# Kernel optimization log

Measured on AMD Instinct MI355X. Metric: run time of the kernel, lower is better.

Reference implementation:

```python
import jax, jax.numpy as jnp
import numpy as np
from jax import lax

BN_EPS = 1e-3  # keras BatchNormalization default
DN = ('NHWC', 'HWIO', 'NHWC')


def setup_inputs() -> dict:
    key = jax.random.key(0)
    ks = jax.random.split(key, 8)
    B, H, W, C = 16, 224, 224, 96
    K = 3
    x = jax.random.normal(ks[0], (B, H, W, C), dtype=jnp.float32)
    dw_kernel = jax.random.normal(ks[1], (K, K, 1, C), dtype=jnp.float32) * 0.1
    dw_bias = jnp.zeros((C,), dtype=jnp.float32)
    pw_kernel = jax.random.normal(ks[2], (1, 1, C, C), dtype=jnp.float32) * 0.1
    pw_bias = jnp.zeros((C,), dtype=jnp.float32)
    gamma = jax.random.uniform(ks[3], (C,), dtype=jnp.float32, minval=0.5, maxval=1.5)
    beta = jax.random.normal(ks[4], (C,), dtype=jnp.float32) * 0.1
    moving_mean = jax.random.normal(ks[5], (C,), dtype=jnp.float32) * 0.1
    moving_var = jax.random.uniform(ks[6], (C,), dtype=jnp.float32, minval=0.5, maxval=1.5)
    return {
        'x': x, 'dw_kernel': dw_kernel, 'dw_bias': dw_bias,
        'pw_kernel': pw_kernel, 'pw_bias': pw_bias,
        'gamma': gamma, 'beta': beta,
        'moving_mean': moving_mean, 'moving_var': moving_var,
    }


def reference(x, dw_kernel, dw_bias, pw_kernel, pw_bias, gamma, beta, moving_mean, moving_var):
    C = x.shape[-1]
    stride = 1
    # ReLU at the start of the op
    y = jax.nn.relu(x)
    # Depthwise conv: feature_group_count = C, kernel HWIO = (K, K, 1, C)
    y = lax.conv_general_dilated(
        y, dw_kernel, window_strides=(stride, stride), padding='SAME',
        dimension_numbers=DN, feature_group_count=C)
    y = y + dw_bias
    # Pointwise 1x1 conv to C_curr channels
    y = lax.conv_general_dilated(
        y, pw_kernel, window_strides=(1, 1), padding='SAME',
        dimension_numbers=DN)
    y = y + pw_bias
    # BatchNormalization (inference mode: use moving statistics)
    inv = gamma * lax.rsqrt(moving_var + BN_EPS)
    y = y * inv + (beta - moving_mean * inv)
    return y
```

## Files before the change

kernel.cpp:

```cpp
#include <hip/hip_runtime.h>
#include <hip/hip_bf16.h>


#define BATCH 16
#define HH 224
#define WWD 224
#define CC 96
#define ROWS (BATCH*HH)
#define TPR 14
#define NTILES (ROWS*TPR)
#define NTHREADS 256
#define WAVES 4
#define NBLOCKS 1024
#define NXCD 8
#define TILES_PER_BAND (NTILES/NXCD)
#define WAVES_PER_BAND ((NBLOCKS/NXCD)*WAVES)
#define PAD 104

typedef __attribute__((ext_vector_type(8))) short short8;
typedef __attribute__((ext_vector_type(4))) float f32x4;

__device__ __forceinline__ unsigned short f2bf(float f){
    union{float f; unsigned u;} v; v.f = f;
    unsigned r = v.u + 0x7fffu + ((v.u >> 16) & 1u);
    return (unsigned short)(r >> 16);
}

__device__ __forceinline__ void tap_fma(const float* __restrict__ xp,
                                        const float* wp,
                                        float acc[3][8])
{
    #pragma unroll
    for (int ks = 0; ks < 3; ++ks) {
        float4 x0 = *reinterpret_cast<const float4*>(xp + ks*32);
        float4 x1 = *reinterpret_cast<const float4*>(xp + ks*32 + 4);
        float4 w0 = *reinterpret_cast<const float4*>(wp + ks*32);
        float4 w1 = *reinterpret_cast<const float4*>(wp + ks*32 + 4);
        acc[ks][0] += fmaxf(x0.x, 0.f) * w0.x;
        acc[ks][1] += fmaxf(x0.y, 0.f) * w0.y;
        acc[ks][2] += fmaxf(x0.z, 0.f) * w0.z;
        acc[ks][3] += fmaxf(x0.w, 0.f) * w0.w;
        acc[ks][4] += fmaxf(x1.x, 0.f) * w1.x;
        acc[ks][5] += fmaxf(x1.y, 0.f) * w1.y;
        acc[ks][6] += fmaxf(x1.z, 0.f) * w1.z;
        acc[ks][7] += fmaxf(x1.w, 0.f) * w1.w;
    }
}

__global__ __launch_bounds__(NTHREADS, 4) void sepconv_kernel(
    const float* __restrict__ x,
    const float* __restrict__ dwk,
    const float* __restrict__ dwb,
    const float* __restrict__ pwk,
    const float* __restrict__ pwb,
    const float* __restrict__ gma,
    const float* __restrict__ bta,
    const float* __restrict__ mmean,
    const float* __restrict__ mvar,
    float* __restrict__ out)
{
    __shared__ __align__(16) unsigned short s_pwT[CC][PAD];
    __shared__ __align__(16) float s_dwk[9][CC];
    __shared__ __align__(16) float s_dwb[CC];
    __shared__ __align__(16) float s_scale[CC];
    __shared__ __align__(16) float s_shift[CC];

    const int t = threadIdx.x;

    for (int e = t; e < CC*CC; e += NTHREADS) {
        int ci = e / CC;
        int co = e - ci*CC;
        s_pwT[co][ci] = f2bf(pwk[e]);
    }
    for (int e = t; e < 9*CC; e += NTHREADS)
        (&s_dwk[0][0])[e] = dwk[e];
    if (t < CC) {
        s_dwb[t] = dwb[t];
        float sc = gma[t] / sqrtf(mvar[t] + 1e-3f);
        s_scale[t] = sc;
        s_shift[t] = (pwb[t] - mmean[t]) * sc + bta[t];
    }
    __syncthreads();

    const int wave = t >> 6;
    const int lane = t & 63;
    const int col  = lane & 15;
    const int quad = lane >> 4;

    float scv[6], shv[6];
    #pragma unroll
    for (int nt = 0; nt < 6; ++nt) {
        scv[nt] = s_scale[nt*16 + col];
        shv[nt] = s_shift[nt*16 + col];
    }

    const int xcd = blockIdx.x & (NXCD-1);
    const int lb  = blockIdx.x >> 3;
    const int gw  = lb*WAVES + wave;
    const int Tend = (xcd+1)*TILES_PER_BAND;

    for (int T = xcd*TILES_PER_BAND + gw; T < Tend; T += WAVES_PER_BAND) {
        const int rrow = T / TPR;
        const int wt   = T - rrow*TPR;
        const int h    = rrow % HH;
        const int w_me = wt*16 + col;
        const float* xb = x + (size_t)(rrow*WWD + w_me)*CC + quad*8;

        float acc[3][8];
        #pragma unroll
        for (int ks = 0; ks < 3; ++ks) {
            float4 b0 = *reinterpret_cast<const float4*>(&s_dwb[ks*32 + quad*8]);
            float4 b1 = *reinterpret_cast<const float4*>(&s_dwb[ks*32 + quad*8 + 4]);
            acc[ks][0]=b0.x; acc[ks][1]=b0.y; acc[ks][2]=b0.z; acc[ks][3]=b0.w;
            acc[ks][4]=b1.x; acc[ks][5]=b1.y; acc[ks][6]=b1.z; acc[ks][7]=b1.w;
        }

        #pragma unroll
        for (int kh = -1; kh <= 1; ++kh) {
            const int h2 = h + kh;
            if ((unsigned)h2 >= HH) continue;
            const float* rp = xb + kh*(WWD*CC);
            const float* wr = &s_dwk[(kh+1)*3][0] + quad*8;
            if (w_me >= 1)       tap_fma(rp - CC, wr,        acc);
                                 tap_fma(rp,      wr + CC,   acc);
            if (w_me <= WWD-2)   tap_fma(rp + CC, wr + 2*CC, acc);
        }

        short8 afr[3];
        #pragma unroll
        for (int ks = 0; ks < 3; ++ks) {
            union { short8 v; unsigned u[4]; } pk;
            #pragma unroll
            for (int j = 0; j < 4; ++j)
                pk.u[j] = (unsigned)f2bf(acc[ks][2*j])
                        | ((unsigned)f2bf(acc[ks][2*j+1]) << 16);
            afr[ks] = pk.v;
        }

        float* ob = out + (size_t)(T*16 + quad*4)*CC + col;
        #pragma unroll
        for (int nt = 0; nt < 6; ++nt) {
            f32x4 macc = {0.f, 0.f, 0.f, 0.f};
            #pragma unroll
            for (int ks = 0; ks < 3; ++ks) {
                short8 bfr = *reinterpret_cast<const short8*>(
                    &s_pwT[nt*16 + col][ks*32 + quad*8]);
                macc = __builtin_amdgcn_mfma_f32_16x16x32_bf16(afr[ks], bfr, macc, 0, 0, 0);
            }
            #pragma unroll
            for (int r2 = 0; r2 < 4; ++r2)
                ob[r2*CC + nt*16] = macc[r2]*scv[nt] + shv[nt];
        }
    }
}

extern "C" void kernel_launch(void* const* d_in, const int* in_sizes, int n_in,
                              void* d_out, int out_size, void* d_ws, size_t ws_size,
                              hipStream_t stream)
{
    sepconv_kernel<<<NBLOCKS, NTHREADS, 0, stream>>>(
        (const float*)d_in[0],
        (const float*)d_in[1],
        (const float*)d_in[2],
        (const float*)d_in[3],
        (const float*)d_in[4],
        (const float*)d_in[5],
        (const float*)d_in[6],
        (const float*)d_in[7],
        (const float*)d_in[8],
        (float*)d_out);
}
```

Measured before the change: 755.6 us.

## Split weight prep into separate kernel and launch one wave per tile

Moves the bf16 transpose of the pointwise weights and the BN scale/shift folding into a small prep kernel that writes to workspace. The main kernel drops its persistent grid-stride loop and launches one block per four tiles, one tile per wave, with occupancy raised to eight blocks per CU. The MFMA operands are swapped so each lane holds four consecutive output channels, which allows float4 stores. Pointwise weights are now read from global memory or cache instead of LDS, which adds global loads per tile, and many more blocks each reload the depthwise weights into LDS.

```diff
diff --git a/kernel.cpp b/kernel.cpp
--- a/kernel.cpp
+++ b/kernel.cpp
@@ -10,12 +10,8 @@
 #define TPR 14
 #define NTILES (ROWS*TPR)
 #define NTHREADS 256
-#define WAVES 4
-#define NBLOCKS 1024
-#define NXCD 8
-#define TILES_PER_BAND (NTILES/NXCD)
-#define WAVES_PER_BAND ((NBLOCKS/NXCD)*WAVES)
-#define PAD 104
+#define NBLOCKS (NTILES/4)
+#define BLK_PER_BAND (NBLOCKS/8)
 
 typedef __attribute__((ext_vector_type(8))) short short8;
 typedef __attribute__((ext_vector_type(4))) float f32x4;
@@ -47,39 +43,43 @@
     }
 }
 
-__global__ __launch_bounds__(NTHREADS, 4) void sepconv_kernel(
+__global__ void sepconv_prep(const float* __restrict__ pwk,
+                             const float* __restrict__ pwb,
+                             const float* __restrict__ gma,
+                             const float* __restrict__ bta,
+                             const float* __restrict__ mmean,
+                             const float* __restrict__ mvar,
+                             unsigned short* __restrict__ pwT,
+                             float* __restrict__ bnsc,
+                             float* __restrict__ bnsh)
+{
+    int e = blockIdx.x*256 + threadIdx.x;
+    int ci = e / CC;
+    int co = e - ci*CC;
+    pwT[co*CC + ci] = f2bf(pwk[e]);
+    if (e < CC) {
+        float sc = gma[e] / sqrtf(mvar[e] + 1e-3f);
+        bnsc[e] = sc;
+        bnsh[e] = (pwb[e] - mmean[e]) * sc + bta[e];
+    }
+}
+
+__global__ __launch_bounds__(NTHREADS, 8) void sepconv_main(
     const float* __restrict__ x,
     const float* __restrict__ dwk,
     const float* __restrict__ dwb,
-    const float* __restrict__ pwk,
-    const float* __restrict__ pwb,
-    const float* __restrict__ gma,
-    const float* __restrict__ bta,
-    const float* __restrict__ mmean,
-    const float* __restrict__ mvar,
+    const unsigned short* __restrict__ pwT,
+    const float* __restrict__ bnsc,
+    const float* __restrict__ bnsh,
     float* __restrict__ out)
 {
-    __shared__ __align__(16) unsigned short s_pwT[CC][PAD];
     __shared__ __align__(16) float s_dwk[9][CC];
     __shared__ __align__(16) float s_dwb[CC];
-    __shared__ __align__(16) float s_scale[CC];
-    __shared__ __align__(16) float s_shift[CC];
 
     const int t = threadIdx.x;
-
-    for (int e = t; e < CC*CC; e += NTHREADS) {
-        int ci = e / CC;
-        int co = e - ci*CC;
-        s_pwT[co][ci] = f2bf(pwk[e]);
-    }
     for (int e = t; e < 9*CC; e += NTHREADS)
         (&s_dwk[0][0])[e] = dwk[e];
-    if (t < CC) {
-        s_dwb[t] = dwb[t];
-        float sc = gma[t] / sqrtf(mvar[t] + 1e-3f);
-        s_scale[t] = sc;
-        s_shift[t] = (pwb[t] - mmean[t]) * sc + bta[t];
-    }
+    if (t < CC) s_dwb[t] = dwb[t];
     __syncthreads();
 
     const int wave = t >> 6;
@@ -87,70 +87,65 @@
     const int col  = lane & 15;
     const int quad = lane >> 4;
 
-    float scv[6], shv[6];
+    const int xcd = blockIdx.x & 7;
+    const int idx = blockIdx.x >> 3;
+    const int T   = (xcd*BLK_PER_BAND + idx)*4 + wave;
+
+    const int rrow = T / TPR;
+    const int wt   = T - rrow*TPR;
+    const int h    = rrow % HH;
+    const int w_me = wt*16 + col;
+    const float* xb = x + (size_t)(rrow*WWD + w_me)*CC + quad*8;
+
+    float acc[3][8];
+    #pragma unroll
+    for (int ks = 0; ks < 3; ++ks) {
+        float4 b0 = *reinterpret_cast<const float4*>(&s_dwb[ks*32 + quad*8]);
+        float4 b1 = *reinterpret_cast<const float4*>(&s_dwb[ks*32 + quad*8 + 4]);
+        acc[ks][0]=b0.x; acc[ks][1]=b0.y; acc[ks][2]=b0.z; acc[ks][3]=b0.w;
+        acc[ks][4]=b1.x; acc[ks][5]=b1.y; acc[ks][6]=b1.z; acc[ks][7]=b1.w;
+    }
+
+    #pragma unroll
+    for (int kh = -1; kh <= 1; ++kh) {
+        const int h2 = h + kh;
+        if ((unsigned)h2 >= HH) continue;
+        const float* rp = xb + kh*(WWD*CC);
+        const float* wr = &s_dwk[(kh+1)*3][0] + quad*8;
+        if (w_me >= 1)       tap_fma(rp - CC, wr,        acc);
+                             tap_fma(rp,      wr + CC,   acc);
+        if (w_me <= WWD-2)   tap_fma(rp + CC, wr + 2*CC, acc);
+    }
+
+    short8 bfr[3];
+    #pragma unroll
+    for (int ks = 0; ks < 3; ++ks) {
+        union { short8 v; unsigned u[4]; } pk;
+        #pragma unroll
+        for (int j = 0; j < 4; ++j)
+            pk.u[j] = (unsigned)f2bf(acc[ks][2*j])
+                    | ((unsigned)f2bf(acc[ks][2*j+1]) << 16);
+        bfr[ks] = pk.v;
+    }
+
+    float* ob = out + (size_t)(T*16 + col)*CC;
     #pragma unroll
     for (int nt = 0; nt < 6; ++nt) {
-        scv[nt] = s_scale[nt*16 + col];
-        shv[nt] = s_shift[nt*16 + col];
-    }
-
-    const int xcd = blockIdx.x & (NXCD-1);
-    const int lb  = blockIdx.x >> 3;
-    const int gw  = lb*WAVES + wave;
-    const int Tend = (xcd+1)*TILES_PER_BAND;
-
-    for (int T = xcd*TILES_PER_BAND + gw; T < Tend; T += WAVES_PER_BAND) {
-        const int rrow = T / TPR;
-        const int wt   = T - rrow*TPR;
-        const int h    = rrow % HH;
-        const int w_me = wt*16 + col;
-        const float* xb = x + (size_t)(rrow*WWD + w_me)*CC + quad*8;
-
-        float acc[3][8];
+        f32x4 macc = {0.f, 0.f, 0.f, 0.f};
         #pragma unroll
         for (int ks = 0; ks < 3; ++ks) {
-            float4 b0 = *reinterpret_cast<const float4*>(&s_dwb[ks*32 + quad*8]);
-            float4 b1 = *reinterpret_cast<const float4*>(&s_dwb[ks*32 + quad*8 + 4]);
-            acc[ks][0]=b0.x; acc[ks][1]=b0.y; acc[ks][2]=b0.z; acc[ks][3]=b0.w;
-            acc[ks][4]=b1.x; acc[ks][5]=b1.y; acc[ks][6]=b1.z; acc[ks][7]=b1.w;
+            short8 pfr = *reinterpret_cast<const short8*>(
+                pwT + (size_t)(nt*16 + col)*CC + ks*32 + quad*8);
+            macc = __builtin_amdgcn_mfma_f32_16x16x32_bf16(pfr, bfr[ks], macc, 0, 0, 0);
         }
-
-        #pragma unroll
-        for (int kh = -1; kh <= 1; ++kh) {
-            const int h2 = h + kh;
-            if ((unsigned)h2 >= HH) continue;
-            const float* rp = xb + kh*(WWD*CC);
-            const float* wr = &s_dwk[(kh+1)*3][0] + quad*8;
-            if (w_me >= 1)       tap_fma(rp - CC, wr,        acc);
-                                 tap_fma(rp,      wr + CC,   acc);
-            if (w_me <= WWD-2)   tap_fma(rp + CC, wr + 2*CC, acc);
-        }
-
-        short8 afr[3];
-        #pragma unroll
-        for (int ks = 0; ks < 3; ++ks) {
-            union { short8 v; unsigned u[4]; } pk;
-            #pragma unroll
-            for (int j = 0; j < 4; ++j)
-                pk.u[j] = (unsigned)f2bf(acc[ks][2*j])
-                        | ((unsigned)f2bf(acc[ks][2*j+1]) << 16);
-            afr[ks] = pk.v;
-        }
-
-        float* ob = out + (size_t)(T*16 + quad*4)*CC + col;
-        #pragma unroll
-        for (int nt = 0; nt < 6; ++nt) {
-            f32x4 macc = {0.f, 0.f, 0.f, 0.f};
-            #pragma unroll
-            for (int ks = 0; ks < 3; ++ks) {
-                short8 bfr = *reinterpret_cast<const short8*>(
-                    &s_pwT[nt*16 + col][ks*32 + quad*8]);
-                macc = __builtin_amdgcn_mfma_f32_16x16x32_bf16(afr[ks], bfr, macc, 0, 0, 0);
-            }
-            #pragma unroll
-            for (int r2 = 0; r2 < 4; ++r2)
-                ob[r2*CC + nt*16] = macc[r2]*scv[nt] + shv[nt];
-        }
+        float4 sc4 = *reinterpret_cast<const float4*>(bnsc + nt*16 + quad*4);
+        float4 sh4 = *reinterpret_cast<const float4*>(bnsh + nt*16 + quad*4);
+        float4 o;
+        o.x = macc[0]*sc4.x + sh4.x;
+        o.y = macc[1]*sc4.y + sh4.y;
+        o.z = macc[2]*sc4.z + sh4.z;
+        o.w = macc[3]*sc4.w + sh4.w;
+        *reinterpret_cast<float4*>(ob + nt*16 + quad*4) = o;
     }
 }
 
@@ -158,15 +153,20 @@
                               void* d_out, int out_size, void* d_ws, size_t ws_size,
                               hipStream_t stream)
 {
-    sepconv_kernel<<<NBLOCKS, NTHREADS, 0, stream>>>(
+    unsigned short* pwT = (unsigned short*)d_ws;
+    float* bnsc = (float*)((char*)d_ws + 9216*2);
+    float* bnsh = bnsc + CC;
+
+    sepconv_prep<<<36, 256, 0, stream>>>(
+        (const float*)d_in[3], (const float*)d_in[4],
+        (const float*)d_in[5], (const float*)d_in[6],
+        (const float*)d_in[7], (const float*)d_in[8],
+        pwT, bnsc, bnsh);
+
+    sepconv_main<<<NBLOCKS, NTHREADS, 0, stream>>>(
         (const float*)d_in[0],
         (const float*)d_in[1],
         (const float*)d_in[2],
-        (const float*)d_in[3],
-        (const float*)d_in[4],
-        (const float*)d_in[5],
-        (const float*)d_in[6],
-        (const float*)d_in[7],
-        (const float*)d_in[8],
+        pwT, bnsc, bnsh,
         (float*)d_out);
 }
```

Result: slower. 849.1 us (+12.4%).
